# Performance work log

Hardware: AMD Instinct MI355X
Metric: run time of the kernel (lower is better)

## Reference

```python
import jax, jax.numpy as jnp
import numpy as np

EPS = 1e-5
BS, NA, NC, NL, NPTS, ED, NG = 1, 900, 6, 4, 13, 256, 8
GD = ED // NG
IMG_W, IMG_H = 704.0, 256.0
FMAP_HW = [(64, 176), (32, 88), (16, 44), (8, 22)]


def _ln(x, g, b):
    m = x.mean(-1, keepdims=True)
    v = ((x - m) ** 2).mean(-1, keepdims=True)
    return (x - m) / jnp.sqrt(v + EPS) * g + b


def _grid_sample(img, grid):
    # img: [N,C,H,W]; grid: [N,P,Q,2] in [-1,1]; bilinear, zeros padding, align_corners=False
    N, C, H, W = img.shape
    gx = jnp.clip((grid[..., 0] + 1.0) * (W * 0.5) - 0.5, -1e4, 1e4)
    gy = jnp.clip((grid[..., 1] + 1.0) * (H * 0.5) - 0.5, -1e4, 1e4)
    x0 = jnp.floor(gx); y0 = jnp.floor(gy)
    wx1 = gx - x0; wy1 = gy - y0; wx0 = 1.0 - wx1; wy0 = 1.0 - wy1
    x0i = x0.astype(jnp.int32); y0i = y0.astype(jnp.int32)
    flat = img.reshape(N, C, H * W)

    def corner(xi, yi, wgt):
        valid = (xi >= 0) & (xi < W) & (yi >= 0) & (yi < H)
        idx = (jnp.clip(yi, 0, H - 1) * W + jnp.clip(xi, 0, W - 1))
        g = jax.vmap(lambda f, i: f[:, i])(flat, idx.reshape(N, -1))  # [N,C,P*Q]
        g = g.reshape(N, C, idx.shape[1], idx.shape[2])
        return g * (wgt * valid)[:, None]

    return (corner(x0i, y0i, wx0 * wy0) + corner(x0i + 1, y0i, wx1 * wy0)
            + corner(x0i, y0i + 1, wx0 * wy1) + corner(x0i + 1, y0i + 1, wx1 * wy1))


def setup_inputs() -> dict:
    key = jax.random.key(0)
    ks = jax.random.split(key, 20)
    d = {}
    d['instance_feature'] = jax.random.normal(ks[0], (BS, NA, ED), jnp.float32)
    xyz = jax.random.normal(ks[1], (BS, NA, 3), jnp.float32) * 1.5
    size = jax.random.normal(ks[2], (BS, NA, 3), jnp.float32) * 0.3
    theta = jax.random.uniform(ks[3], (BS, NA, 1), jnp.float32) * (2.0 * np.pi)
    vel = jax.random.normal(ks[4], (BS, NA, 3), jnp.float32) * 0.1
    d['anchor'] = jnp.concatenate([xyz, size, jnp.sin(theta), jnp.cos(theta), vel], -1)
    d['anchor_embed'] = jax.random.normal(ks[5], (BS, NA, ED), jnp.float32)
    for i, (h, w) in enumerate(FMAP_HW):
        d[f'fmap{i}'] = jax.random.normal(ks[6 + i], (BS, NC, ED, h, w), jnp.float32)
    base = jnp.array([[80., 0., 0., 352.], [0., 80., 0., 128.],
                      [0., 0., 0., 1.], [0., 0., 0., 1.]], jnp.float32)
    proj = jnp.tile(base, (BS, NC, 1, 1))
    proj = proj.at[:, :, :2, :].add(jax.random.normal(ks[10], (BS, NC, 2, 4), jnp.float32) * 2.0)
    d['projection_mat'] = proj
    d['image_wh'] = jnp.broadcast_to(jnp.array([IMG_W, IMG_H], jnp.float32), (BS, NC, 2))
    d['fix_scale'] = jnp.array([[0, 0, 0], [0.45, 0, 0], [-0.45, 0, 0], [0, 0.45, 0],
                                [0, -0.45, 0], [0, 0, 0.45], [0, 0, -0.45]], jnp.float32)

    def w(k, shape):
        return jax.random.normal(k, shape, jnp.float32) * 0.02

    d['lfc_w'] = w(ks[11], (ED, 6 * 3)); d['lfc_b'] = jnp.zeros((18,), jnp.float32)
    d['cam_w1'] = w(ks[12], (12, ED)); d['cam_b1'] = jnp.zeros((ED,), jnp.float32)
    d['cam_g1'] = jnp.ones((ED,), jnp.float32); d['cam_be1'] = jnp.zeros((ED,), jnp.float32)
    d['cam_w2'] = w(ks[13], (ED, ED)); d['cam_b2'] = jnp.zeros((ED,), jnp.float32)
    d['cam_g2'] = jnp.ones((ED,), jnp.float32); d['cam_be2'] = jnp.zeros((ED,), jnp.float32)
    d['wfc_w'] = w(ks[14], (ED, NG * NL * NPTS)); d['wfc_b'] = jnp.zeros((NG * NL * NPTS,), jnp.float32)
    d['op_w'] = w(ks[15], (ED, ED)); d['op_b'] = jnp.zeros((ED,), jnp.float32)
    return d


def reference(instance_feature, anchor, anchor_embed, fmap0, fmap1, fmap2, fmap3,
              projection_mat, image_wh, fix_scale, lfc_w, lfc_b,
              cam_w1, cam_b1, cam_g1, cam_be1, cam_w2, cam_b2, cam_g2, cam_be2,
              wfc_w, wfc_b, op_w, op_b):
    bs, na = instance_feature.shape[:2]
    # ---- keypoint generation ----
    size = jnp.exp(anchor[..., None, 3:6])                       # [bs,na,1,3]
    kp = fix_scale * size                                        # [bs,na,7,3]
    ls = jax.nn.sigmoid(instance_feature @ lfc_w + lfc_b).reshape(bs, na, -1, 3) - 0.5
    kp = jnp.concatenate([kp, ls * size], axis=-2)               # [bs,na,NPTS,3]
    sin, cos = anchor[..., 6:7], anchor[..., 7:8]                # [bs,na,1]
    kx, ky, kz = kp[..., 0], kp[..., 1], kp[..., 2]
    key_points = jnp.stack([cos * kx - sin * ky, sin * kx + cos * ky, kz], -1) \
                 + anchor[..., None, 0:3]                        # [bs,na,NPTS,3]
    # ---- per-cam/level/point group weights ----
    feat = instance_feature + anchor_embed
    cam_in = projection_mat[:, :, :3].reshape(bs, NC, 12)
    h = jax.nn.relu(cam_in @ cam_w1 + cam_b1); h = _ln(h, cam_g1, cam_be1)
    h = jax.nn.relu(h @ cam_w2 + cam_b2); cam_embed = _ln(h, cam_g2, cam_be2)
    f = feat[:, :, None] + cam_embed[:, None]                    # [bs,na,NC,ED]
    wts = (f @ wfc_w + wfc_b).reshape(bs, na, NC * NL * NPTS, NG)
    wts = jax.nn.softmax(wts, axis=-2).reshape(bs, na, NC, NL, NPTS, NG)
    # ---- multi-cam projection + bilinear sampling ----
    pts = jnp.concatenate([key_points, jnp.ones_like(key_points[..., :1])], -1)
    p2d = jnp.einsum('bcij,banj->bcani', projection_mat, pts)    # [bs,NC,na,NPTS,4]
    p2d = p2d[..., :2] / jnp.maximum(p2d[..., 2:3], 1e-5)
    p2d = p2d / image_wh[:, :, None, None]
    grid = (p2d * 2.0 - 1.0).reshape(bs * NC, na, NPTS, 2)
    feats = jnp.stack([_grid_sample(fm.reshape(bs * NC, ED, fm.shape[-2], fm.shape[-1]), grid)
                       for fm in (fmap0, fmap1, fmap2, fmap3)], axis=1)  # [bs*NC,NL,ED,na,NPTS]
    feats = feats.reshape(bs, NC, NL, ED, na, NPTS).transpose(0, 4, 1, 2, 5, 3)  # [bs,na,NC,NL,NPTS,ED]
    # ---- group-weighted fusion over cams & levels, then sum over points ----
    fg = feats.reshape(bs, na, NC, NL, NPTS, NG, GD)
    fused = jnp.einsum('bnclpg,bnclpgd->bnpgd', wts, fg).reshape(bs, na, NPTS, ED)
    fused = fused.sum(axis=2)                                    # [bs,na,ED]
    out = fused @ op_w + op_b
    return jnp.concatenate([out, instance_feature], axis=-1)     # [bs,na,2*ED]
```

## Files before the change

### kernel.cpp

```cpp
#include <hip/hip_runtime.h>
#include <stdint.h>

#define NA 900
#define NC 6
#define NL 4
#define NPTS 13
#define ED 256
#define NG 8
#define LNEPS 1e-5f
#define NSTAGE 718303
#define NSTAGE_BLOCKS 2806
#define NTRANS 5616
#define NCOPY 672
#define NSAMP 312
#define LGS 313

struct PIn { const void* p[24]; };

__device__ __forceinline__ float b2f(unsigned short u){
  union { uint32_t i; float f; } v; v.i = ((uint32_t)u)<<16; return v.f;
}
__device__ __forceinline__ unsigned short f2b(float f){
  union { float f; uint32_t i; } v; v.f = f;
  uint32_t r = v.i + 0x7FFFu + ((v.i>>16)&1u);
  return (unsigned short)(r>>16);
}
#define BLO(u) __uint_as_float((u)<<16)
#define BHI(u) __uint_as_float((u)&0xffff0000u)

__device__ __forceinline__ float ldx(const void* p, int i, bool bf){
  return bf ? b2f(((const unsigned short*)p)[i]) : ((const float*)p)[i];
}

__device__ __forceinline__ bool sniff_bf(const unsigned short* __restrict__ u16){
  int lane = threadIdx.x & 63;
  unsigned short u = u16[2*lane];
  int e = (u>>7)&0xFF;
  int sane = (e>=110 && e<=135) ? 1 : 0;
  #pragma unroll
  for (int m=32;m;m>>=1) sane += __shfl_xor(sane, m);
  return sane >= 48;
}

__device__ __forceinline__ void blockReduce2(float& a, float& b, float* lds){
  #pragma unroll
  for (int m=32;m;m>>=1){ a += __shfl_xor(a,m); b += __shfl_xor(b,m); }
  int w = threadIdx.x>>6;
  if ((threadIdx.x&63)==0){ lds[w]=a; lds[w+4]=b; }
  __syncthreads();
  a = lds[0]+lds[1]+lds[2]+lds[3];
  b = lds[4]+lds[5]+lds[6]+lds[7];
  __syncthreads();
}

__global__ __launch_bounds__(256) void k_prep(PIn in, float* __restrict__ stage,
                                              unsigned short* __restrict__ tf,
                                              unsigned short* __restrict__ wfcw_h,
                                              unsigned short* __restrict__ opw_h,
                                              float* __restrict__ Bc){
  const bool bf = sniff_bf((const unsigned short*)in.p[0]);
  const int tid = threadIdx.x;
  int b = blockIdx.x;

  __shared__ unsigned short T[64][68];
  __shared__ float h[ED];
  __shared__ float cE[ED];
  __shared__ float red8[8];
  __shared__ float part[4][64];

  if (b < NSTAGE_BLOCKS){
    const int cum[21] = {0,230400,240300,470700,470796,470808,470829,475437,475455,
                         478527,478783,479039,479295,544831,545087,545343,545599,
                         652095,652511,718047,718303};
    const int map[20] = {0,1,2,7,8,9,10,11,12,13,14,15,16,17,18,19,20,21,22,23};
    int idx = b*256 + tid;
    if (idx >= NSTAGE) return;
    int seg = 0, base = 0;
    #pragma unroll
    for (int s=1;s<20;s++) if (idx >= cum[s]){ seg = s; base = cum[s]; }
    const void* src = in.p[map[0]];
    #pragma unroll
    for (int s=1;s<20;s++) if (seg==s) src = in.p[map[s]];
    stage[idx] = ldx(src, idx - base, bf);
    return;
  }
  b -= NSTAGE_BLOCKS;
  if (b < NTRANS){
    const int xb[4]  = {176,44,11,3};
    const int HWs[4] = {11264,2816,704,176};
    const int TFO[4] = {0,17301504,21626880,22708224};
    int l, local;
    if      (b < 4224){ l=0; local=b;      }
    else if (b < 5280){ l=1; local=b-4224; }
    else if (b < 5544){ l=2; local=b-5280; }
    else              { l=3; local=b-5544; }
    int pt = local % xb[l]; int rest = local / xb[l];
    int ct = rest & 3; int c = rest >> 2;
    const int HW = HWs[l];
    const int px0 = pt*64;
    const void* src = in.p[3+l];
    #pragma unroll
    for (int p=0;p<2;p++){
      int lch = p*32 + (tid>>3);
      int gch = ct*64 + lch;
      int pxv = (tid&7)*8;
      size_t base = (size_t)(c*ED+gch)*HW + px0 + pxv;
      unsigned short v[8];
      if (px0 + pxv + 8 <= HW){
        if (bf){
          uint4 q = *reinterpret_cast<const uint4*>((const unsigned short*)src + base);
          v[0]=q.x&0xffff; v[1]=q.x>>16; v[2]=q.y&0xffff; v[3]=q.y>>16;
          v[4]=q.z&0xffff; v[5]=q.z>>16; v[6]=q.w&0xffff; v[7]=q.w>>16;
        } else {
          float4 f0 = *reinterpret_cast<const float4*>((const float*)src + base);
          float4 f1 = *reinterpret_cast<const float4*>((const float*)src + base + 4);
          v[0]=f2b(f0.x); v[1]=f2b(f0.y); v[2]=f2b(f0.z); v[3]=f2b(f0.w);
          v[4]=f2b(f1.x); v[5]=f2b(f1.y); v[6]=f2b(f1.z); v[7]=f2b(f1.w);
        }
      } else {
        #pragma unroll
        for (int i=0;i<8;i++){
          int px = px0+pxv+i;
          v[i] = (px<HW) ? (bf ? ((const unsigned short*)src)[base+i]
                               : f2b(((const float*)src)[base+i])) : (unsigned short)0;
        }
      }
      #pragma unroll
      for (int i=0;i<8;i++) T[pxv+i][lch] = v[i];
    }
    __syncthreads();
    unsigned short* dst = tf + TFO[l] + (size_t)c*HW*ED + ct*64;
    #pragma unroll
    for (int p=0;p<2;p++){
      int pxl = p*32 + (tid>>3);
      int px = px0 + pxl;
      if (px >= HW) continue;
      int ch8 = (tid&7)*8;
      ushort4 lo = *reinterpret_cast<ushort4*>(&T[pxl][ch8]);
      ushort4 hi = *reinterpret_cast<ushort4*>(&T[pxl][ch8+4]);
      union { ushort4 hh[2]; uint4 q; } u;
      u.hh[0]=lo; u.hh[1]=hi;
      *reinterpret_cast<uint4*>(dst + (size_t)px*ED + ch8) = u.q;
    }
    return;
  }
  b -= NTRANS;
  if (b < NCOPY){
    int idx = b*256 + tid;
    if (idx < 106496){
      wfcw_h[idx] = bf ? ((const unsigned short*)in.p[20])[idx]
                       : f2b(((const float*)in.p[20])[idx]);
    } else {
      int j = idx - 106496;
      opw_h[j] = bf ? ((const unsigned short*)in.p[22])[j]
                    : f2b(((const float*)in.p[22])[j]);
    }
    return;
  }
  b -= NCOPY;
  {
    const void* proj = in.p[7];
    const void* w1 = in.p[12]; const void* b1 = in.p[13];
    const void* g1 = in.p[14]; const void* be1 = in.p[15];
    const void* w2 = in.p[16]; const void* b2 = in.p[17];
    const void* g2 = in.p[18]; const void* be2 = in.p[19];
    const void* wfcw = in.p[20]; const void* wfcb = in.p[21];
    const int c = b/7, colt = b - (b/7)*7;
    float ci[12];
    #pragma unroll
    for (int i=0;i<12;i++) ci[i] = ldx(proj, c*16+i, bf);
    float acc = ldx(b1, tid, bf);
    #pragma unroll
    for (int k=0;k<12;k++) acc += ci[k]*ldx(w1, k*ED+tid, bf);
    float x = fmaxf(acc, 0.f);
    float s=x, q=x*x;
    blockReduce2(s,q,red8);
    float mean = s*(1.f/ED), var = q*(1.f/ED)-mean*mean;
    h[tid] = (x-mean)*rsqrtf(var+LNEPS)*ldx(g1,tid,bf) + ldx(be1,tid,bf);
    __syncthreads();
    acc = ldx(b2, tid, bf);
    #pragma unroll 8
    for (int k=0;k<ED;k++) acc += h[k]*ldx(w2, k*ED+tid, bf);
    x = fmaxf(acc,0.f);
    s=x; q=x*x;
    blockReduce2(s,q,red8);
    mean = s*(1.f/ED); var = q*(1.f/ED)-mean*mean;
    cE[tid] = (x-mean)*rsqrtf(var+LNEPS)*ldx(g2,tid,bf) + ldx(be2,tid,bf);
    __syncthreads();
    const int kc = tid>>6, colL = tid&63, col = colt*64+colL;
    float a = 0.f;
    if (col < 416){
      #pragma unroll 8
      for (int k=0;k<64;k++) a += cE[kc*64+k]*ldx(wfcw, (kc*64+k)*416+col, bf);
    }
    part[kc][colL] = a;
    __syncthreads();
    if (kc==0 && col<416)
      Bc[c*416+col] = part[0][colL]+part[1][colL]+part[2][colL]+part[3][colL] + ldx(wfcb,col,bf);
  }
}

__global__ __launch_bounds__(512, 8) void k_anchor(
    const float* __restrict__ stage, const unsigned short* __restrict__ tf,
    const unsigned short* __restrict__ wfcw_h, const unsigned short* __restrict__ opw_h,
    const float* __restrict__ Bc, const void* __restrict__ rawinst,
    void* __restrict__ outv){
  const int n = blockIdx.x, tid = threadIdx.x;
  const bool bf = sniff_bf((const unsigned short*)rawinst);

  const float* s_inst = stage + 0;
  const float* s_anc  = stage + 230400;
  const float* s_ae   = stage + 240300;
  const float* s_proj = stage + 470700;
  const float* s_imwh = stage + 470796;
  const float* s_fixs = stage + 470808;
  const float* s_lw   = stage + 470829;
  const float* s_lb   = stage + 475437;
  const float* s_opb  = stage + 718047;

  __shared__ float ifs[ED];
  __shared__ float fe[ED];
  __shared__ float lg2[8*LGS];
  __shared__ uint4 cbi[NSAMP];
  __shared__ uint4 cwf[NSAMP];
  __shared__ unsigned short coff[NSAMP];
  __shared__ float red[16][ED+4];
  __shared__ float fu[ED];
  __shared__ float kp[13][3];
  __shared__ float sc[8];
  __shared__ float lsv[18];
  __shared__ int scnt;

  if (tid < 256){
    float iv = s_inst[n*ED+tid];
    ifs[tid] = iv;
    fe[tid]  = iv + s_ae[n*ED+tid];
  } else {
    int t = tid - 256;
    if (t == 0)      scnt = 0;
    if (t < 3)       sc[t] = s_anc[n*11+t];
    else if (t == 3) sc[3] = s_anc[n*11+6];
    else if (t == 4) sc[4] = s_anc[n*11+7];
    else if (t < 8)  sc[t] = __expf(s_anc[n*11+t-2]);
  }
  __syncthreads();
  if (tid < 144){
    int d = tid>>3, j = tid&7;
    float a = 0.f;
    #pragma unroll 8
    for (int k=j*32;k<j*32+32;k++) a += ifs[k]*s_lw[k*18+d];
    a += __shfl_xor(a,1); a += __shfl_xor(a,2); a += __shfl_xor(a,4);
    if (j==0){
      a += s_lb[d];
      lsv[d] = 1.f/(1.f+__expf(-a)) - 0.5f;
    }
  }
  __syncthreads();
  if (tid < 13){
    float kx,ky,kz;
    if (tid < 7){
      kx = s_fixs[tid*3+0]*sc[5];
      ky = s_fixs[tid*3+1]*sc[6];
      kz = s_fixs[tid*3+2]*sc[7];
    } else {
      int j = tid-7;
      kx = lsv[j*3+0]*sc[5]; ky = lsv[j*3+1]*sc[6]; kz = lsv[j*3+2]*sc[7];
    }
    kp[tid][0] = sc[4]*kx - sc[3]*ky + sc[0];
    kp[tid][1] = sc[3]*kx + sc[4]*ky + sc[1];
    kp[tid][2] = kz + sc[2];
  }
  if (tid < 416){
    float a0 = 0.f;
    #pragma unroll 8
    for (int k=0;k<ED;k++) a0 += fe[k]*b2f(wfcw_h[k*416+tid]);
    const int g = tid & 7, rr = tid >> 3;
    #pragma unroll
    for (int c=0;c<NC;c++)
      lg2[g*LGS + c*52 + rr] = a0 + Bc[c*416+tid];
  }
  __syncthreads();
  if (tid < NSAMP){
    int s = tid;
    int c = s/52, rr = s - c*52;
    int l = rr/13, p = rr - l*13;
    float m[12];
    #pragma unroll
    for (int i=0;i<12;i++) m[i] = s_proj[c*16+i];
    float X=kp[p][0], Y=kp[p][1], Z=kp[p][2];
    float x = m[0]*X + m[1]*Y + m[2]*Z  + m[3];
    float y = m[4]*X + m[5]*Y + m[6]*Z  + m[7];
    float z = m[8]*X + m[9]*Y + m[10]*Z + m[11];
    float d = fmaxf(z, 1e-5f);
    float px = x/(d*s_imwh[c*2+0]), py = y/(d*s_imwh[c*2+1]);
    const int W = 176>>l, H = 64>>l;
    const int TFO[4] = {0,17301504,21626880,22708224};
    float gx = fminf(fmaxf(px*(float)W - 0.5f, -10000.f), 10000.f);
    float gy = fminf(fmaxf(py*(float)H - 0.5f, -10000.f), 10000.f);
    float xf = floorf(gx), yf = floorf(gy);
    int x0 = (int)xf, y0 = (int)yf;
    float wx1 = gx-xf, wy1 = gy-yf;
    float wx0 = 1.f-wx1, wy0 = 1.f-wy1;
    bool vx0 = (x0>=0)&&(x0<W),   vx1 = (x0+1>=0)&&(x0+1<W);
    bool vy0 = (y0>=0)&&(y0<H),   vy1 = (y0+1>=0)&&(y0+1<H);
    float w00 = (vx0&&vy0) ? wx0*wy0 : 0.f;
    float w10 = (vx1&&vy0) ? wx1*wy0 : 0.f;
    float w01 = (vx0&&vy1) ? wx0*wy1 : 0.f;
    float w11 = (vx1&&vy1) ? wx1*wy1 : 0.f;
    if (w00+w10+w01+w11 != 0.f){
      int cx0 = min(max(x0,0),W-1), cx1 = min(max(x0+1,0),W-1);
      int cy0 = min(max(y0,0),H-1), cy1 = min(max(y0+1,0),H-1);
      uint32_t cam = (uint32_t)TFO[l] + (uint32_t)(c*H*W)*ED;
      uint4 bi, wv;
      bi.x = cam + (uint32_t)(cy0*W+cx0)*ED;
      bi.y = cam + (uint32_t)(cy0*W+cx1)*ED;
      bi.z = cam + (uint32_t)(cy1*W+cx0)*ED;
      bi.w = cam + (uint32_t)(cy1*W+cx1)*ED;
      wv.x = __float_as_uint(w00); wv.y = __float_as_uint(w10);
      wv.z = __float_as_uint(w01); wv.w = __float_as_uint(w11);
      int slot = atomicAdd(&scnt, 1);
      cbi[slot] = bi;
      cwf[slot] = wv;
      coff[slot] = (unsigned short)s;
    }
  }
  {
    const int g = tid>>6, j = tid&63;
    float v[5]; float mx = -1e30f;
    #pragma unroll
    for (int i=0;i<5;i++){
      int e = j + 64*i;
      float val = -1e30f;
      if (e < NSAMP){
        val = lg2[g*LGS + e];
        mx = fmaxf(mx, val);
      }
      v[i] = val;
    }
    #pragma unroll
    for (int mk=32;mk;mk>>=1) mx = fmaxf(mx, __shfl_xor(mx, mk));
    float sum = 0.f;
    #pragma unroll
    for (int i=0;i<5;i++){
      if (j + 64*i < NSAMP){ float ex = __expf(v[i]-mx); v[i] = ex; sum += ex; }
    }
    #pragma unroll
    for (int mk=32;mk;mk>>=1) sum += __shfl_xor(sum, mk);
    float inv = 1.f/sum;
    #pragma unroll
    for (int i=0;i<5;i++){
      int e = j + 64*i;
      if (e < NSAMP) lg2[g*LGS + e] = v[i]*inv;
    }
  }
  __syncthreads();
  {
    const int m = scnt;
    const int strm = tid>>5, lane32 = tid&31;
    const int ch8 = lane32*8, gg = lane32>>2;
    float acc[8] = {0,0,0,0,0,0,0,0};
    int i = strm;
    for (; i + 16 < m; i += 32){
      uint4 biA = cbi[i],    wfA = cwf[i];
      uint4 biB = cbi[i+16], wfB = cwf[i+16];
      float wgA = lg2[gg*LGS + coff[i]],  wgB = lg2[gg*LGS + coff[i+16]];
      uint4 a00 = *reinterpret_cast<const uint4*>(tf + biA.x + ch8);
      uint4 a10 = *reinterpret_cast<const uint4*>(tf + biA.y + ch8);
      uint4 a01 = *reinterpret_cast<const uint4*>(tf + biA.z + ch8);
      uint4 a11 = *reinterpret_cast<const uint4*>(tf + biA.w + ch8);
      uint4 b00 = *reinterpret_cast<const uint4*>(tf + biB.x + ch8);
      uint4 b10 = *reinterpret_cast<const uint4*>(tf + biB.y + ch8);
      uint4 b01 = *reinterpret_cast<const uint4*>(tf + biB.z + ch8);
      uint4 b11 = *reinterpret_cast<const uint4*>(tf + biB.w + ch8);
      float pA00 = wgA*__uint_as_float(wfA.x), pA10 = wgA*__uint_as_float(wfA.y);
      float pA01 = wgA*__uint_as_float(wfA.z), pA11 = wgA*__uint_as_float(wfA.w);
      float pB00 = wgB*__uint_as_float(wfB.x), pB10 = wgB*__uint_as_float(wfB.y);
      float pB01 = wgB*__uint_as_float(wfB.z), pB11 = wgB*__uint_as_float(wfB.w);
      acc[0] += pA00*BLO(a00.x)+pA10*BLO(a10.x)+pA01*BLO(a01.x)+pA11*BLO(a11.x)
              + pB00*BLO(b00.x)+pB10*BLO(b10.x)+pB01*BLO(b01.x)+pB11*BLO(b11.x);
      acc[1] += pA00*BHI(a00.x)+pA10*BHI(a10.x)+pA01*BHI(a01.x)+pA11*BHI(a11.x)
              + pB00*BHI(b00.x)+pB10*BHI(b10.x)+pB01*BHI(b01.x)+pB11*BHI(b11.x);
      acc[2] += pA00*BLO(a00.y)+pA10*BLO(a10.y)+pA01*BLO(a01.y)+pA11*BLO(a11.y)
              + pB00*BLO(b00.y)+pB10*BLO(b10.y)+pB01*BLO(b01.y)+pB11*BLO(b11.y);
      acc[3] += pA00*BHI(a00.y)+pA10*BHI(a10.y)+pA01*BHI(a01.y)+pA11*BHI(a11.y)
              + pB00*BHI(b00.y)+pB10*BHI(b10.y)+pB01*BHI(b01.y)+pB11*BHI(b11.y);
      acc[4] += pA00*BLO(a00.z)+pA10*BLO(a10.z)+pA01*BLO(a01.z)+pA11*BLO(a11.z)
              + pB00*BLO(b00.z)+pB10*BLO(b10.z)+pB01*BLO(b01.z)+pB11*BLO(b11.z);
      acc[5] += pA00*BHI(a00.z)+pA10*BHI(a10.z)+pA01*BHI(a01.z)+pA11*BHI(a11.z)
              + pB00*BHI(b00.z)+pB10*BHI(b10.z)+pB01*BHI(b01.z)+pB11*BHI(b11.z);
      acc[6] += pA00*BLO(a00.w)+pA10*BLO(a10.w)+pA01*BLO(a01.w)+pA11*BLO(a11.w)
              + pB00*BLO(b00.w)+pB10*BLO(b10.w)+pB01*BLO(b01.w)+pB11*BLO(b11.w);
      acc[7] += pA00*BHI(a00.w)+pA10*BHI(a10.w)+pA01*BHI(a01.w)+pA11*BHI(a11.w)
              + pB00*BHI(b00.w)+pB10*BHI(b10.w)+pB01*BHI(b01.w)+pB11*BHI(b11.w);
    }
    for (; i < m; i += 16){
      uint4 bi = cbi[i], wf = cwf[i];
      float wg = lg2[gg*LGS + coff[i]];
      uint4 q00 = *reinterpret_cast<const uint4*>(tf + bi.x + ch8);
      uint4 q10 = *reinterpret_cast<const uint4*>(tf + bi.y + ch8);
      uint4 q01 = *reinterpret_cast<const uint4*>(tf + bi.z + ch8);
      uint4 q11 = *reinterpret_cast<const uint4*>(tf + bi.w + ch8);
      float p00 = wg*__uint_as_float(wf.x), p10 = wg*__uint_as_float(wf.y);
      float p01 = wg*__uint_as_float(wf.z), p11 = wg*__uint_as_float(wf.w);
      acc[0] += p00*BLO(q00.x)+p10*BLO(q10.x)+p01*BLO(q01.x)+p11*BLO(q11.x);
      acc[1] += p00*BHI(q00.x)+p10*BHI(q10.x)+p01*BHI(q01.x)+p11*BHI(q11.x);
      acc[2] += p00*BLO(q00.y)+p10*BLO(q10.y)+p01*BLO(q01.y)+p11*BLO(q11.y);
      acc[3] += p00*BHI(q00.y)+p10*BHI(q10.y)+p01*BHI(q01.y)+p11*BHI(q11.y);
      acc[4] += p00*BLO(q00.z)+p10*BLO(q10.z)+p01*BLO(q01.z)+p11*BLO(q11.z);
      acc[5] += p00*BHI(q00.z)+p10*BHI(q10.z)+p01*BHI(q01.z)+p11*BHI(q11.z);
      acc[6] += p00*BLO(q00.w)+p10*BLO(q10.w)+p01*BLO(q01.w)+p11*BLO(q11.w);
      acc[7] += p00*BHI(q00.w)+p10*BHI(q10.w)+p01*BHI(q01.w)+p11*BHI(q11.w);
    }
    *reinterpret_cast<float4*>(&red[strm][ch8])   = make_float4(acc[0],acc[1],acc[2],acc[3]);
    *reinterpret_cast<float4*>(&red[strm][ch8+4]) = make_float4(acc[4],acc[5],acc[6],acc[7]);
  }
  __syncthreads();
  if (tid < 256){
    float r = 0.f;
    #pragma unroll
    for (int i=0;i<16;i++) r += red[i][tid];
    fu[tid] = r;
  }
  __syncthreads();
  {
    const int col = tid & 255, half = tid >> 8;
    const int k0 = half*128;
    float a = 0.f;
    #pragma unroll 8
    for (int k=k0;k<k0+128;k++) a += fu[k]*b2f(opw_h[k*ED+col]);
    red[half][col] = a;
  }
  __syncthreads();
  {
    float v;
    if (tid < 256) v = s_opb[tid] + red[0][tid] + red[1][tid];
    else           v = ifs[tid-256];
    if (bf) ((unsigned short*)outv)[n*512+tid] = f2b(v);
    else    ((float*)outv)[n*512+tid]          = v;
  }
}

extern "C" void kernel_launch(void* const* d_in, const int* in_sizes, int n_in,
                              void* d_out, int out_size, void* d_ws, size_t ws_size,
                              hipStream_t stream){
  char* ws = (char*)d_ws;
  size_t off = 0;
  auto alloc = [&](size_t bytes)->char*{
    char* p = ws + off; off += (bytes + 63) & ~size_t(63); return p;
  };
  unsigned short* tf = (unsigned short*)alloc((size_t)22978560*2);
  float* stage  = (float*)alloc((size_t)NSTAGE*4);
  unsigned short* wfcw_h = (unsigned short*)alloc((size_t)106496*2);
  unsigned short* opw_h  = (unsigned short*)alloc((size_t)65536*2);
  float* Bc     = (float*)alloc((size_t)NC*416*4);

  PIn in;
  for (int i=0;i<24;i++) in.p[i] = d_in[i];

  k_prep<<<NSTAGE_BLOCKS + NTRANS + NCOPY + 42, 256, 0, stream>>>(in, stage, tf, wfcw_h, opw_h, Bc);
  k_anchor<<<NA, 512, 0, stream>>>(stage, tf, wfcw_h, opw_h, Bc, d_in[0], d_out);
}
```

Baseline: 247.0 us.

## Widen feature-map transpose tiles to 256 pixels with XOR-swizzled LDS and batched loads

The transpose section of the prep kernel now gives each block 256 pixels instead of 64, so there are 1416 transpose blocks instead of 5616. For bf16 input, all 128-bit loads are issued up front. The unpadded LDS tile uses an XOR swizzle in place of padding, so both the write and the 16-byte read side avoid bank conflicts. Launch bounds for k_anchor are also relaxed from 8 to 4 waves per EU, which trades occupancy for more registers per thread.

```diff
diff --git a/kernel.cpp b/kernel.cpp
--- a/kernel.cpp
+++ b/kernel.cpp
@@ -10,7 +10,7 @@
 #define LNEPS 1e-5f
 #define NSTAGE 718303
 #define NSTAGE_BLOCKS 2806
-#define NTRANS 5616
+#define NTRANS 1416
 #define NCOPY 672
 #define NSAMP 312
 #define LGS 313
@@ -62,7 +62,7 @@
   const int tid = threadIdx.x;
   int b = blockIdx.x;
 
-  __shared__ unsigned short T[64][68];
+  __shared__ unsigned short TT[64][64];
   __shared__ float h[ED];
   __shared__ float cE[ED];
   __shared__ float red8[8];
@@ -86,61 +86,82 @@
   }
   b -= NSTAGE_BLOCKS;
   if (b < NTRANS){
-    const int xb[4]  = {176,44,11,3};
-    const int HWs[4] = {11264,2816,704,176};
-    const int TFO[4] = {0,17301504,21626880,22708224};
+    const int tiles[4] = {44,11,3,1};
+    const int HWs[4]   = {11264,2816,704,176};
+    const int TFO[4]   = {0,17301504,21626880,22708224};
     int l, local;
-    if      (b < 4224){ l=0; local=b;      }
-    else if (b < 5280){ l=1; local=b-4224; }
-    else if (b < 5544){ l=2; local=b-5280; }
-    else              { l=3; local=b-5544; }
-    int pt = local % xb[l]; int rest = local / xb[l];
+    if      (b < 1056){ l=0; local=b;      }
+    else if (b < 1320){ l=1; local=b-1056; }
+    else if (b < 1392){ l=2; local=b-1320; }
+    else              { l=3; local=b-1392; }
+    int pt = local % tiles[l]; int rest = local / tiles[l];
     int ct = rest & 3; int c = rest >> 2;
     const int HW = HWs[l];
-    const int px0 = pt*64;
+    const int px0 = pt*256;
     const void* src = in.p[3+l];
-    #pragma unroll
-    for (int p=0;p<2;p++){
-      int lch = p*32 + (tid>>3);
-      int gch = ct*64 + lch;
-      int pxv = (tid&7)*8;
-      size_t base = (size_t)(c*ED+gch)*HW + px0 + pxv;
-      unsigned short v[8];
-      if (px0 + pxv + 8 <= HW){
-        if (bf){
-          uint4 q = *reinterpret_cast<const uint4*>((const unsigned short*)src + base);
-          v[0]=q.x&0xffff; v[1]=q.x>>16; v[2]=q.y&0xffff; v[3]=q.y>>16;
-          v[4]=q.z&0xffff; v[5]=q.z>>16; v[6]=q.w&0xffff; v[7]=q.w>>16;
-        } else {
-          float4 f0 = *reinterpret_cast<const float4*>((const float*)src + base);
-          float4 f1 = *reinterpret_cast<const float4*>((const float*)src + base + 4);
-          v[0]=f2b(f0.x); v[1]=f2b(f0.y); v[2]=f2b(f0.z); v[3]=f2b(f0.w);
-          v[4]=f2b(f1.x); v[5]=f2b(f1.y); v[6]=f2b(f1.z); v[7]=f2b(f1.w);
+    const int j8 = tid & 7;
+    const int w8 = tid >> 3;
+
+    uint4 v[2][4];
+    if (bf){
+      #pragma unroll
+      for (int p=0;p<2;p++){
+        int ch = ct*64 + p*32 + w8;
+        size_t rowb = (size_t)(c*ED+ch)*HW;
+        #pragma unroll
+        for (int q=0;q<4;q++){
+          int pxs = px0 + q*64 + j8*8;
+          if (pxs < HW)
+            v[p][q] = *reinterpret_cast<const uint4*>((const unsigned short*)src + rowb + pxs);
+          else
+            v[p][q] = make_uint4(0,0,0,0);
         }
-      } else {
+      }
+    }
+    for (int q=0;q<4;q++){
+      if (px0 + q*64 >= HW) break;
+      if (!bf){
         #pragma unroll
-        for (int i=0;i<8;i++){
-          int px = px0+pxv+i;
-          v[i] = (px<HW) ? (bf ? ((const unsigned short*)src)[base+i]
-                               : f2b(((const float*)src)[base+i])) : (unsigned short)0;
+        for (int p=0;p<2;p++){
+          int ch = ct*64 + p*32 + w8;
+          size_t rowb = (size_t)(c*ED+ch)*HW;
+          int pxs = px0 + q*64 + j8*8;
+          if (pxs < HW){
+            float4 f0 = *reinterpret_cast<const float4*>((const float*)src + rowb + pxs);
+            float4 f1 = *reinterpret_cast<const float4*>((const float*)src + rowb + pxs + 4);
+            v[p][q].x = (uint32_t)f2b(f0.x) | ((uint32_t)f2b(f0.y)<<16);
+            v[p][q].y = (uint32_t)f2b(f0.z) | ((uint32_t)f2b(f0.w)<<16);
+            v[p][q].z = (uint32_t)f2b(f1.x) | ((uint32_t)f2b(f1.y)<<16);
+            v[p][q].w = (uint32_t)f2b(f1.z) | ((uint32_t)f2b(f1.w)<<16);
+          } else v[p][q] = make_uint4(0,0,0,0);
         }
       }
       #pragma unroll
-      for (int i=0;i<8;i++) T[pxv+i][lch] = v[i];
-    }
-    __syncthreads();
-    unsigned short* dst = tf + TFO[l] + (size_t)c*HW*ED + ct*64;
-    #pragma unroll
-    for (int p=0;p<2;p++){
-      int pxl = p*32 + (tid>>3);
-      int px = px0 + pxl;
-      if (px >= HW) continue;
-      int ch8 = (tid&7)*8;
-      ushort4 lo = *reinterpret_cast<ushort4*>(&T[pxl][ch8]);
-      ushort4 hi = *reinterpret_cast<ushort4*>(&T[pxl][ch8+4]);
-      union { ushort4 hh[2]; uint4 q; } u;
-      u.hh[0]=lo; u.hh[1]=hi;
-      *reinterpret_cast<uint4*>(dst + (size_t)px*ED + ch8) = u.q;
+      for (int p=0;p<2;p++){
+        int r = p*32 + w8;
+        int g8 = (j8 ^ (r>>3))<<3;
+        *reinterpret_cast<uint4*>(&TT[r][g8]) = v[p][q];
+      }
+      __syncthreads();
+      #pragma unroll
+      for (int p=0;p<2;p++){
+        int pxl = p*32 + w8;
+        int px  = px0 + q*64 + pxl;
+        int colq = (((pxl>>3) ^ j8)<<3) | (pxl & 7);
+        int rb = j8*8;
+        unsigned short t0 = TT[rb+0][colq], t1 = TT[rb+1][colq];
+        unsigned short t2 = TT[rb+2][colq], t3 = TT[rb+3][colq];
+        unsigned short t4 = TT[rb+4][colq], t5 = TT[rb+5][colq];
+        unsigned short t6 = TT[rb+6][colq], t7 = TT[rb+7][colq];
+        uint4 o;
+        o.x = (uint32_t)t0 | ((uint32_t)t1<<16);
+        o.y = (uint32_t)t2 | ((uint32_t)t3<<16);
+        o.z = (uint32_t)t4 | ((uint32_t)t5<<16);
+        o.w = (uint32_t)t6 | ((uint32_t)t7<<16);
+        if (px < HW)
+          *reinterpret_cast<uint4*>(tf + TFO[l] + (size_t)c*HW*ED + (size_t)px*ED + ct*64 + j8*8) = o;
+      }
+      __syncthreads();
     }
     return;
   }
@@ -200,7 +221,7 @@
   }
 }
 
-__global__ __launch_bounds__(512, 8) void k_anchor(
+__global__ __launch_bounds__(512, 4) void k_anchor(
     const float* __restrict__ stage, const unsigned short* __restrict__ tf,
     const unsigned short* __restrict__ wfcw_h, const unsigned short* __restrict__ opw_h,
     const float* __restrict__ Bc, const void* __restrict__ rawinst,
```

Result: slower. 253.9 us (+2.8%).
